# Kernel tuning notes

Hardware: AMD Instinct MI355X
Metric: run time of the kernel (lower is better)

Reference implementation:

```python
import jax, jax.numpy as jnp
import numpy as np


def _conv2d(x, w, b, dilation=1):
    pad = dilation * (w.shape[-1] // 2)
    y = jax.lax.conv_general_dilated(x, w, (1, 1), [(pad, pad), (pad, pad)],
                                     rhs_dilation=(dilation, dilation),
                                     dimension_numbers=("NCHW", "OIHW", "NCHW"))
    return y + b[None, :, None, None]


def _bn(x, gamma, beta, mean, var):
    # eval-mode BatchNorm2d, eps=1e-5
    inv = gamma / jnp.sqrt(var + 1e-5)
    return (x - mean[None, :, None, None]) * inv[None, :, None, None] + beta[None, :, None, None]


def _frft2d(x, angles):
    # Faithful port of the source frft2d, including the quirk that
    # temp[shft, :] indexes the BATCH dim: since shft is a permutation of
    # 0..N-1, the net effect is that batch entries 0..N-1 get (i)fft'd along
    # axis -2 and entries >= N are untouched.
    temp = jnp.swapaxes(x, -1, -2)
    BC = temp.shape[0]
    for a in angles:
        a = a % 4
        N = temp.shape[-2]
        sN = np.float32(np.sqrt(N))
        mask = (jnp.arange(BC) < N)[:, None, None]
        if a == 1:
            temp = jnp.where(mask, jnp.fft.fft(temp, axis=-2) / sN, temp)
        elif a == 2:
            temp = jnp.flip(temp, axis=-2)
        elif a == 3:
            temp = jnp.where(mask, jnp.fft.ifft(temp, axis=-2) * sN, temp)
        temp = jnp.swapaxes(temp, -1, -2)
    return temp


def setup_inputs() -> dict:
    key = jax.random.key(0)
    ks = jax.random.split(key, 12)
    B, C, H, W = 4, 64, 256, 256
    f = lambda k, shape, s=0.1: jax.random.normal(k, shape, dtype=jnp.float32) * s
    z1 = jnp.zeros((1,), jnp.float32)
    o1 = jnp.ones((1,), jnp.float32)
    return {
        "x": jax.random.normal(ks[0], (B, C, H, W), dtype=jnp.float32),
        "kernel_map": jnp.ones((H, W), dtype=jnp.float32),
        "theta_w": f(ks[1], (1, 1, 3, 3)), "theta_b": z1,
        "phase_w": f(ks[2], (1, 1, 3, 3)), "phase_b": z1,
        "phase_gamma": o1, "phase_beta": z1, "phase_mean": z1, "phase_var": o1,
        "amp_w": f(ks[3], (1, 1, 1, 1)), "amp_b": z1,
        "ms_w1": f(ks[4], (1, 1, 3, 3)), "ms_b1": z1,
        "ms_w2": f(ks[5], (1, 1, 3, 3)), "ms_b2": z1,
        "ms_w3": f(ks[6], (1, 1, 3, 3)), "ms_b3": z1,
        "fc1_w": f(ks[7], (16, 1)), "fc1_b": jnp.zeros((16,), jnp.float32),
        "fc2_w": f(ks[8], (1, 16)), "fc2_b": z1,
        "fin_w": f(ks[9], (1, 6, 1, 1)), "fin_b": z1,
        "fin_gamma": o1, "fin_beta": z1, "fin_mean": z1, "fin_var": o1,
    }


def reference(x, kernel_map, theta_w, theta_b, phase_w, phase_b,
              phase_gamma, phase_beta, phase_mean, phase_var,
              amp_w, amp_b, ms_w1, ms_b1, ms_w2, ms_b2, ms_w3, ms_b3,
              fc1_w, fc1_b, fc2_w, fc2_b, fin_w, fin_b,
              fin_gamma, fin_beta, fin_mean, fin_var):
    B, C, H, W = x.shape
    BC = B * C
    xf = x.reshape(BC, H, W)
    trker = jnp.clip(jax.nn.softplus(kernel_map), 1e-3, 10.0)
    # Riesz kernels, p=(1,1) => sin(pi/2)
    Y = (jnp.arange(H, dtype=jnp.float32) + 1.0)[:, None]
    X = (jnp.arange(W, dtype=jnp.float32) + 1.0)[None, :]
    sa = np.float32(np.sin(0.5 * np.pi))
    denom = jnp.sqrt((X / sa) ** 2 + (Y / sa) ** 2) + 1e-6
    dx = ((-1j) * (X / sa) / denom).astype(jnp.complex64) * trker
    dy = ((-1j) * (Y / sa) / denom).astype(jnp.complex64) * trker
    fa = _frft2d(xf.astype(jnp.complex64), [1, 1])
    R1 = jnp.abs(_frft2d(dx * fa, [-1, -1])) + 1e-6
    R2 = jnp.abs(_frft2d(dy * fa, [-1, -1])) + 1e-6
    A = jnp.sqrt(jax.nn.relu(xf ** 2 + R1 ** 2 + R2 ** 2) + 1e-6)[:, None]
    P = jnp.arctan2(jnp.sqrt(R1 ** 2 + R2 ** 2) + 1e-6, xf + 1e-6)[:, None]
    theta = jnp.arctan2(R2, R1 + 1e-6)[:, None]
    G_theta = theta * jax.nn.sigmoid(_conv2d(theta, theta_w, theta_b))
    P_prime = jax.nn.relu(_bn(_conv2d(P, phase_w, phase_b),
                              phase_gamma, phase_beta, phase_mean, phase_var))
    A_boost = A + jax.nn.relu(_conv2d(A, amp_w, amp_b))
    ms = jnp.concatenate([_conv2d(A_boost, ms_w1, ms_b1, 1),
                          _conv2d(A_boost, ms_w2, ms_b2, 2),
                          _conv2d(A_boost, ms_w3, ms_b3, 3)], axis=1)
    # adaptive_avg_pool2d to (H, W) is the identity here
    gf = jnp.mean(A_boost, axis=(2, 3))  # (BC, 1)
    gw = jax.nn.sigmoid(jax.nn.relu(gf @ fc1_w.T + fc1_b) @ fc2_w.T + fc2_b)
    gw = gw[:, :, None, None]  # (BC,1,1,1)
    fusion = jnp.concatenate([A_boost, P_prime, G_theta, ms * gw], axis=1)  # (BC,6,H,W)
    fused = _bn(_conv2d(fusion, fin_w, fin_b), fin_gamma, fin_beta, fin_mean, fin_var)
    fused = jnp.clip(jax.nn.relu(fused), 0.0, 1.0)
    return fused.reshape(B, C, H, W)
```

## Files before the change

### kernel.cpp

```cpp
#include <hip/hip_runtime.h>
#include <hip/hip_fp16.h>
#include <math.h>

#define PI_F 3.14159265358979323846f

__device__ __forceinline__ unsigned dr4(unsigned n){
  return ((n & 3u) << 6) | (((n >> 2) & 3u) << 4) | (((n >> 4) & 3u) << 2) | ((n >> 6) & 3u);
}

__device__ __forceinline__ float2 cmul(float2 a, float2 b){
  return make_float2(a.x * b.x - a.y * b.y, a.x * b.y + a.y * b.x);
}

__device__ __forceinline__ void fill_tw256(float2* tw, int tid){
  float s, c;
  sincosf((2.0f * PI_F / 256.0f) * (float)tid, &s, &c);
  tw[tid] = make_float2(c, s);
  __syncthreads();
}

template<bool INV>
__device__ __forceinline__ void bfly4(float2 a, float2 b, float2 c, float2 d,
                                      float2 w1, float2 w2, float2 w3,
                                      float2& X0, float2& X1, float2& X2, float2& X3){
  if (!INV){ w1.y = -w1.y; w2.y = -w2.y; w3.y = -w3.y; }
  const float2 t1 = cmul(b, w1), t2 = cmul(c, w2), t3 = cmul(d, w3);
  const float2 s0 = make_float2(a.x + t2.x, a.y + t2.y);
  const float2 s1 = make_float2(a.x - t2.x, a.y - t2.y);
  const float2 s2 = make_float2(t1.x + t3.x, t1.y + t3.y);
  const float2 s3 = make_float2(t1.x - t3.x, t1.y - t3.y);
  X0 = make_float2(s0.x + s2.x, s0.y + s2.y);
  X2 = make_float2(s0.x - s2.x, s0.y - s2.y);
  if (!INV){
    X1 = make_float2(s1.x + s3.y, s1.y - s3.x);
    X3 = make_float2(s1.x - s3.y, s1.y + s3.x);
  } else {
    X1 = make_float2(s1.x - s3.y, s1.y + s3.x);
    X3 = make_float2(s1.x + s3.y, s1.y - s3.x);
  }
}

template<bool INV, bool DUAL>
__device__ __forceinline__ void fft256_row(float2* A, float2* B, const float2* tw, int lane){
  #pragma unroll
  for (int s = 0; s < 4; ++s){
    const int q = 1 << (2 * s);
    const int m = 64 >> (2 * s);
    const int p = lane & (q - 1);
    const int base = ((lane >> (2 * s)) << (2 * s + 2)) + p;
    const float2 w1 = tw[p * m], w2 = tw[2 * p * m], w3 = tw[3 * p * m];
    {
      float2 X0, X1, X2, X3;
      bfly4<INV>(A[base], A[base + q], A[base + 2 * q], A[base + 3 * q], w1, w2, w3, X0, X1, X2, X3);
      A[base] = X0; A[base + q] = X1; A[base + 2 * q] = X2; A[base + 3 * q] = X3;
    }
    if (DUAL){
      float2 X0, X1, X2, X3;
      bfly4<INV>(B[base], B[base + q], B[base + 2 * q], B[base + 3 * q], w1, w2, w3, X0, X1, X2, X3);
      B[base] = X0; B[base + q] = X1; B[base + 2 * q] = X2; B[base + 3 * q] = X3;
    }
    __syncthreads();
  }
}

template<bool INV>
__device__ __forceinline__ void fft256_cols(float2* buf, const float2* tw, int c, int sub){
  #pragma unroll
  for (int s = 0; s < 4; ++s){
    const int q = 1 << (2 * s);
    const int m = 64 >> (2 * s);
    #pragma unroll
    for (int k = 0; k < 2; ++k){
      const int t = sub + (k << 5);
      const int p = t & (q - 1);
      const int base = ((t >> (2 * s)) << (2 * s + 2)) + p;
      const float2 w1 = tw[p * m], w2 = tw[2 * p * m], w3 = tw[3 * p * m];
      float2 X0, X1, X2, X3;
      bfly4<INV>(buf[base * 9 + c], buf[(base + q) * 9 + c],
                 buf[(base + 2 * q) * 9 + c], buf[(base + 3 * q) * 9 + c],
                 w1, w2, w3, X0, X1, X2, X3);
      buf[base * 9 + c] = X0; buf[(base + q) * 9 + c] = X1;
      buf[(base + 2 * q) * 9 + c] = X2; buf[(base + 3 * q) * 9 + c] = X3;
    }
    __syncthreads();
  }
}

__device__ __forceinline__ float packh2(float re, float im){
  __half2 h = __floats2half2_rn(re, im);
  return __builtin_bit_cast(float, h);
}
__device__ __forceinline__ float2 unpackh2(float p){
  return __half22float2(__builtin_bit_cast(__half2, p));
}
__device__ __forceinline__ unsigned packh2u(float a, float b){
  return __builtin_bit_cast(unsigned, __floats2half2_rn(a, b));
}

#define PLANE_PITCH 264
#define PLANE_ELEMS (264 * 264)

__global__ __launch_bounds__(256) void k0_prep(const float* __restrict__ km, float* __restrict__ sT){
  const int idx = blockIdx.x * 256 + threadIdx.x;
  const int u = idx >> 8, v = idx & 255;
  const float kv = km[idx];
  float sp = fmaxf(kv, 0.f) + log1pf(expf(-fabsf(kv)));
  sp = fminf(fmaxf(sp, 1e-3f), 10.f);
  const float fu = (float)(u + 1), fv = (float)(v + 1);
  sT[v * 256 + u] = sp / (sqrtf(fu * fu + fv * fv) + 1e-6f) * (1.0f / 65536.0f);
}

__global__ __launch_bounds__(256) void k1_row(const float* __restrict__ xs, float2* __restrict__ SPEC){
  __shared__ float2 tw[256];
  __shared__ __align__(16) float2 buf[4][256];
  const int tid = threadIdx.x;
  fill_tw256(tw, tid);
  const int grp = tid >> 6, lane = tid & 63;
  const int rs = blockIdx.x * 4 + grp;
  const int j0 = lane << 2;
  const float4 xv = *(const float4*)(xs + (size_t)rs * 256 + j0);
  float2* rb = buf[grp];
  rb[dr4(j0 + 0)] = make_float2(xv.x, 0.f);
  rb[dr4(j0 + 1)] = make_float2(xv.y, 0.f);
  rb[dr4(j0 + 2)] = make_float2(xv.z, 0.f);
  rb[dr4(j0 + 3)] = make_float2(xv.w, 0.f);
  __syncthreads();
  fft256_row<false, false>(rb, (float2*)nullptr, tw, lane);
  float4* dst = (float4*)(SPEC + (size_t)rs * 256);
  const float4* src = (const float4*)rb;
  dst[lane * 2]     = src[lane * 2];
  dst[lane * 2 + 1] = src[lane * 2 + 1];
}

__global__ __launch_bounds__(256) void k2_col(float2* SPEC, const float* __restrict__ sT){
  __shared__ float2 tw[256];
  __shared__ float2 bufA[256 * 9];
  __shared__ float2 bufB[256 * 9];
  const int tid = threadIdx.x;
  fill_tw256(tw, tid);
  const int b_local = blockIdx.x >> 5;
  const int u0 = (blockIdx.x & 31) << 3;
  const int c = tid & 7, sub = tid >> 3;
  const size_t rowbase = (size_t)b_local * 256;

  #pragma unroll
  for (int k = 0; k < 8; ++k){
    const int l = tid + (k << 8);
    const int r = l >> 3, cc = l & 7;
    bufA[dr4(r) * 9 + cc] = SPEC[(rowbase + r) * 256 + u0 + cc];
  }
  __syncthreads();
  fft256_cols<false>(bufA, tw, c, sub);

  float s8[8];
  #pragma unroll
  for (int k = 0; k < 8; ++k){
    const int l = tid + (k << 8);
    const int v = l >> 3, cc = l & 7;
    const int u = u0 + cc;
    const float s = sT[v * 256 + u];
    s8[k] = s;
    const float2 F = bufA[v * 9 + cc];
    const float s1 = (float)(v + 1) * s;
    bufB[dr4(v) * 9 + cc] = make_float2(s1 * F.y, -s1 * F.x);
  }
  __syncthreads();
  fft256_cols<true>(bufB, tw, c, sub);

  float u1h[8];
  #pragma unroll
  for (int k = 0; k < 8; ++k){
    const int l = tid + (k << 8);
    const int i = l >> 3, cc = l & 7;
    const float2 f1 = bufB[i * 9 + cc];
    u1h[k] = packh2(f1.x, f1.y);
  }
  __syncthreads();

  #pragma unroll
  for (int k = 0; k < 8; ++k){
    const int l = tid + (k << 8);
    const int v = l >> 3, cc = l & 7;
    const int u = u0 + cc;
    const float2 F = bufA[v * 9 + cc];
    const float s2 = (float)(u + 1) * s8[k];
    bufB[dr4(v) * 9 + cc] = make_float2(s2 * F.y, -s2 * F.x);
  }
  __syncthreads();
  fft256_cols<true>(bufB, tw, c, sub);

  #pragma unroll
  for (int k = 0; k < 8; ++k){
    const int l = tid + (k << 8);
    const int i = l >> 3, cc = l & 7;
    const float2 f2 = bufB[i * 9 + cc];
    float2 slot;
    slot.x = u1h[k];
    slot.y = packh2(f2.x, f2.y);
    SPEC[(rowbase + i) * 256 + u0 + cc] = slot;
  }
}

__global__ __launch_bounds__(256) void k3_rowinv(const float* __restrict__ xs,
    const float2* __restrict__ SPEC, float* __restrict__ Ap, unsigned* __restrict__ PTp,
    const float* __restrict__ ampw, const float* __restrict__ ampb){
  __shared__ float2 tw[256];
  __shared__ __align__(16) float2 b1[4][256];
  __shared__ __align__(16) float2 b2[4][256];
  const int tid = threadIdx.x;
  fill_tw256(tw, tid);
  const int grp = tid >> 6, lane = tid & 63;
  const int rs = blockIdx.x * 4 + grp;
  const int j0 = lane << 2;
  const float4* srow = (const float4*)(SPEC + (size_t)rs * 256);
  const float4 qa = srow[lane * 2], qb = srow[lane * 2 + 1];
  b1[grp][dr4(j0 + 0)] = unpackh2(qa.x); b2[grp][dr4(j0 + 0)] = unpackh2(qa.y);
  b1[grp][dr4(j0 + 1)] = unpackh2(qa.z); b2[grp][dr4(j0 + 1)] = unpackh2(qa.w);
  b1[grp][dr4(j0 + 2)] = unpackh2(qb.x); b2[grp][dr4(j0 + 2)] = unpackh2(qb.y);
  b1[grp][dr4(j0 + 3)] = unpackh2(qb.z); b2[grp][dr4(j0 + 3)] = unpackh2(qb.w);
  __syncthreads();
  fft256_row<true, true>(b1[grp], b2[grp], tw, lane);

  const float aw = *ampw, ab = *ampb;
  const float4 xv = *(const float4*)(xs + (size_t)rs * 256 + j0);
  const float xa[4] = {xv.x, xv.y, xv.z, xv.w};
  float A4[4], P4[4], T4[4];
  #pragma unroll
  for (int k = 0; k < 4; ++k){
    const float2 r1 = b1[grp][j0 + k];
    const float2 r2 = b2[grp][j0 + k];
    const float R1 = sqrtf(r1.x * r1.x + r1.y * r1.y) + 1e-6f;
    const float R2 = sqrtf(r2.x * r2.x + r2.y * r2.y) + 1e-6f;
    const float xvv = xa[k];
    const float A = sqrtf(fmaxf(xvv * xvv + R1 * R1 + R2 * R2, 0.f) + 1e-6f);
    P4[k] = atan2f(sqrtf(R1 * R1 + R2 * R2) + 1e-6f, xvv + 1e-6f);
    T4[k] = atan2f(R2, R1 + 1e-6f);
    A4[k] = A + fmaxf(aw * A + ab, 0.f);
  }
  const int img = rs >> 8, i = rs & 255;
  float* arow = Ap + (size_t)img * PLANE_ELEMS + (size_t)(i + 4) * PLANE_PITCH + 4;
  *(float4*)(arow + j0) = make_float4(A4[0], A4[1], A4[2], A4[3]);
  unsigned* ptrow = PTp + (size_t)img * PLANE_ELEMS + (size_t)(i + 4) * PLANE_PITCH + 4;
  uint4 pk;
  pk.x = packh2u(P4[0], T4[0]); pk.y = packh2u(P4[1], T4[1]);
  pk.z = packh2u(P4[2], T4[2]); pk.w = packh2u(P4[3], T4[3]);
  *(uint4*)(ptrow + j0) = pk;
}

__global__ __launch_bounds__(256) void kpad(float* __restrict__ Ap, unsigned* __restrict__ PTp){
  const int b = blockIdx.x, tid = threadIdx.x;
  float* A = Ap + (size_t)b * PLANE_ELEMS;
  unsigned* P = PTp + (size_t)b * PLANE_ELEMS;
  for (int idx = tid; idx < 4 * PLANE_PITCH; idx += 256){
    const int r = idx / PLANE_PITCH, c2 = idx % PLANE_PITCH;
    A[r * PLANE_PITCH + c2] = 0.f;          P[r * PLANE_PITCH + c2] = 0u;
    A[(260 + r) * PLANE_PITCH + c2] = 0.f;  P[(260 + r) * PLANE_PITCH + c2] = 0u;
  }
  for (int idx = tid; idx < 256 * 4; idx += 256){
    const int r = 4 + (idx >> 2), c2 = idx & 3;
    A[r * PLANE_PITCH + c2] = 0.f;          P[r * PLANE_PITCH + c2] = 0u;
    A[r * PLANE_PITCH + 260 + c2] = 0.f;    P[r * PLANE_PITCH + 260 + c2] = 0u;
  }
}

__global__ __launch_bounds__(256) void k4_gw(const float* __restrict__ Ap,
    const float* __restrict__ fc1w, const float* __restrict__ fc1b,
    const float* __restrict__ fc2w, const float* __restrict__ fc2b,
    float* __restrict__ gw){
  __shared__ float red[256];
  const int b = blockIdx.x, tid = threadIdx.x;
  const float4* row = (const float4*)(Ap + (size_t)b * PLANE_ELEMS + (size_t)(tid + 4) * PLANE_PITCH + 4);
  float s = 0.f;
  #pragma unroll 8
  for (int k = 0; k < 64; ++k){
    const float4 v = row[k];
    s += v.x + v.y + v.z + v.w;
  }
  red[tid] = s;
  __syncthreads();
  #pragma unroll
  for (int off = 128; off; off >>= 1){
    if (tid < off) red[tid] += red[tid + off];
    __syncthreads();
  }
  if (tid == 0){
    const float gf = red[0] * (1.0f / 65536.0f);
    float acc = fc2b[0];
    #pragma unroll
    for (int k = 0; k < 16; ++k)
      acc += fc2w[k] * fmaxf(gf * fc1w[k] + fc1b[k], 0.f);
    gw[b] = 1.f / (1.f + expf(-acc));
  }
}

__global__ __launch_bounds__(256) void k5_fuse(
    const float* __restrict__ Ap, const unsigned* __restrict__ PTp,
    const float* __restrict__ gwp,
    const float* __restrict__ theta_w, const float* __restrict__ theta_b,
    const float* __restrict__ phase_w, const float* __restrict__ phase_b,
    const float* __restrict__ phase_gamma, const float* __restrict__ phase_beta,
    const float* __restrict__ phase_mean, const float* __restrict__ phase_var,
    const float* __restrict__ ms_w1, const float* __restrict__ ms_b1,
    const float* __restrict__ ms_w2, const float* __restrict__ ms_b2,
    const float* __restrict__ ms_w3, const float* __restrict__ ms_b3,
    const float* __restrict__ fin_w, const float* __restrict__ fin_b,
    const float* __restrict__ fin_gamma, const float* __restrict__ fin_beta,
    const float* __restrict__ fin_mean, const float* __restrict__ fin_var,
    float* __restrict__ out){
  const int z = blockIdx.z;
  const int tx = threadIdx.x & 15, ty = threadIdx.x >> 4;
  const int j0 = (blockIdx.x << 6) + (tx << 2);
  const int i0 = (blockIdx.y << 6) + (ty << 2);
  const float* Abase = Ap + (size_t)z * PLANE_ELEMS;
  const unsigned* Pbase = PTp + (size_t)z * PLANE_ELEMS;

  float tw9[9], pw9[9], w1[9], w2[9], w3[9];
  #pragma unroll
  for (int k = 0; k < 9; ++k){
    tw9[k] = theta_w[k]; pw9[k] = phase_w[k];
    w1[k] = ms_w1[k]; w2[k] = ms_w2[k]; w3[k] = ms_w3[k];
  }
  const float b1s = ms_b1[0], b2s = ms_b2[0], b3s = ms_b3[0];
  const float tbs = theta_b[0], pbs = phase_b[0];

  float4 m1[4], m2[4], m3[4], at[4], ap[4], Ac[4], Tc[4];
  #pragma unroll
  for (int oi = 0; oi < 4; ++oi){
    m1[oi] = make_float4(b1s, b1s, b1s, b1s);
    m2[oi] = make_float4(b2s, b2s, b2s, b2s);
    m3[oi] = make_float4(b3s, b3s, b3s, b3s);
    at[oi] = make_float4(tbs, tbs, tbs, tbs);
    ap[oi] = make_float4(pbs, pbs, pbs, pbs);
  }

  #pragma unroll
  for (int lr = 0; lr < 10; ++lr){
    const int ar = i0 - 3 + lr;
    const float* rowp = Abase + (size_t)(ar + 4) * PLANE_PITCH + j0;
    const float4 va = *(const float4*)(rowp);
    const float4 vb = *(const float4*)(rowp + 4);
    const float4 vc = *(const float4*)(rowp + 8);
    const float a[12] = {va.x, va.y, va.z, va.w, vb.x, vb.y, vb.z, vb.w, vc.x, vc.y, vc.z, vc.w};
    #pragma unroll
    for (int oi = 0; oi < 4; ++oi){
      const int dd = lr - 3 - oi;
      if (dd >= -1 && dd <= 1){
        const int wr = (dd + 1) * 3;
        #pragma unroll
        for (int dx = -1; dx <= 1; ++dx){
          const float w = w1[wr + dx + 1];
          m1[oi].x += w * a[4 + 0 + dx]; m1[oi].y += w * a[4 + 1 + dx];
          m1[oi].z += w * a[4 + 2 + dx]; m1[oi].w += w * a[4 + 3 + dx];
        }
      }
      if (dd == -2 || dd == 0 || dd == 2){
        const int wr = (dd / 2 + 1) * 3;
        #pragma unroll
        for (int dx = -1; dx <= 1; ++dx){
          const float w = w2[wr + dx + 1];
          m2[oi].x += w * a[4 + 0 + 2 * dx]; m2[oi].y += w * a[4 + 1 + 2 * dx];
          m2[oi].z += w * a[4 + 2 + 2 * dx]; m2[oi].w += w * a[4 + 3 + 2 * dx];
        }
      }
      if (dd == -3 || dd == 0 || dd == 3){
        const int wr = (dd / 3 + 1) * 3;
        #pragma unroll
        for (int dx = -1; dx <= 1; ++dx){
          const float w = w3[wr + dx + 1];
          m3[oi].x += w * a[4 + 0 + 3 * dx]; m3[oi].y += w * a[4 + 1 + 3 * dx];
          m3[oi].z += w * a[4 + 2 + 3 * dx]; m3[oi].w += w * a[4 + 3 + 3 * dx];
        }
      }
      if (dd == 0) Ac[oi] = make_float4(a[4], a[5], a[6], a[7]);
    }
  }

  #pragma unroll
  for (int lr = 0; lr < 6; ++lr){
    const int ar = i0 - 1 + lr;
    const unsigned* rowp = Pbase + (size_t)(ar + 4) * PLANE_PITCH + j0;
    const uint4 ua = *(const uint4*)(rowp);
    const uint4 ub = *(const uint4*)(rowp + 4);
    const uint4 uc = *(const uint4*)(rowp + 8);
    const unsigned uu[12] = {ua.x, ua.y, ua.z, ua.w, ub.x, ub.y, ub.z, ub.w, uc.x, uc.y, uc.z, uc.w};
    float p[12], t[12];
    #pragma unroll
    for (int k = 0; k < 12; ++k){
      const float2 pt = __half22float2(__builtin_bit_cast(__half2, uu[k]));
      p[k] = pt.x; t[k] = pt.y;
    }
    #pragma unroll
    for (int oi = 0; oi < 4; ++oi){
      const int dd = lr - 1 - oi;
      if (dd >= -1 && dd <= 1){
        const int wr = (dd + 1) * 3;
        #pragma unroll
        for (int dx = -1; dx <= 1; ++dx){
          const float wp = pw9[wr + dx + 1], wt = tw9[wr + dx + 1];
          ap[oi].x += wp * p[4 + 0 + dx]; ap[oi].y += wp * p[4 + 1 + dx];
          ap[oi].z += wp * p[4 + 2 + dx]; ap[oi].w += wp * p[4 + 3 + dx];
          at[oi].x += wt * t[4 + 0 + dx]; at[oi].y += wt * t[4 + 1 + dx];
          at[oi].z += wt * t[4 + 2 + dx]; at[oi].w += wt * t[4 + 3 + dx];
        }
      }
      if (dd == 0) Tc[oi] = make_float4(t[4], t[5], t[6], t[7]);
    }
  }

  const float gwb = gwp[z];
  const float inv_p = phase_gamma[0] * rsqrtf(phase_var[0] + 1e-5f);
  const float pmean = phase_mean[0], pbeta = phase_beta[0];
  const float f0 = fin_w[0], f1 = fin_w[1], f2 = fin_w[2];
  const float f3 = fin_w[3], f4 = fin_w[4], f5 = fin_w[5];
  const float fb = fin_b[0];
  const float inv_f = fin_gamma[0] * rsqrtf(fin_var[0] + 1e-5f);
  const float fmean = fin_mean[0], fbeta = fin_beta[0];

  #pragma unroll
  for (int oi = 0; oi < 4; ++oi){
    float o4[4];
    const float mm1[4] = {m1[oi].x, m1[oi].y, m1[oi].z, m1[oi].w};
    const float mm2[4] = {m2[oi].x, m2[oi].y, m2[oi].z, m2[oi].w};
    const float mm3[4] = {m3[oi].x, m3[oi].y, m3[oi].z, m3[oi].w};
    const float tt[4]  = {at[oi].x, at[oi].y, at[oi].z, at[oi].w};
    const float pp[4]  = {ap[oi].x, ap[oi].y, ap[oi].z, ap[oi].w};
    const float ac[4]  = {Ac[oi].x, Ac[oi].y, Ac[oi].z, Ac[oi].w};
    const float tc[4]  = {Tc[oi].x, Tc[oi].y, Tc[oi].z, Tc[oi].w};
    #pragma unroll
    for (int oj = 0; oj < 4; ++oj){
      const float Gt = tc[oj] / (1.f + expf(-tt[oj]));
      const float Pp = fmaxf((pp[oj] - pmean) * inv_p + pbeta, 0.f);
      const float pre = f0 * ac[oj] + f1 * Pp + f2 * Gt
                      + gwb * (f3 * mm1[oj] + f4 * mm2[oj] + f5 * mm3[oj]) + fb;
      float o = (pre - fmean) * inv_f + fbeta;
      o4[oj] = fminf(fmaxf(o, 0.f), 1.f);
    }
    *(float4*)(out + ((size_t)(z * 256 + i0 + oi) << 8) + j0) = make_float4(o4[0], o4[1], o4[2], o4[3]);
  }
}

extern "C" void kernel_launch(void* const* d_in, const int* in_sizes, int n_in,
                              void* d_out, int out_size, void* d_ws, size_t ws_size,
                              hipStream_t stream){
  const float* x  = (const float*)d_in[0];
  const float* km = (const float*)d_in[1];

  int N = 1;
  while (N < 64){
    const size_t need = (size_t)(256 / N) * 1081856ull + 262144ull + 1024ull;
    if (need <= ws_size) break;
    N <<= 1;
  }
  const int imgsPer = 256 / N;
  const int rowsPer = imgsPer * 256;

  char* ws = (char*)d_ws;
  float*    Aplane = (float*)ws;
  unsigned* PTplane = (unsigned*)(ws + (size_t)imgsPer * 278784ull);
  float2*   SPEC   = (float2*)(ws + (size_t)imgsPer * 557568ull);
  float*    sTab   = (float*)(ws + (size_t)imgsPer * 1081856ull);
  float*    gwbuf  = (float*)(ws + (size_t)imgsPer * 1081856ull + 262144ull);

  k0_prep<<<256, 256, 0, stream>>>(km, sTab);

  for (int s = 0; s < N; ++s){
    const float* xs = x + (size_t)s * rowsPer * 256;
    float* outs = (float*)d_out + (size_t)s * rowsPer * 256;

    k1_row<<<rowsPer / 4, 256, 0, stream>>>(xs, SPEC);
    k2_col<<<imgsPer * 32, 256, 0, stream>>>(SPEC, sTab);
    k3_rowinv<<<rowsPer / 4, 256, 0, stream>>>(xs, SPEC, Aplane, PTplane,
        (const float*)d_in[10], (const float*)d_in[11]);
    kpad<<<imgsPer, 256, 0, stream>>>(Aplane, PTplane);
    k4_gw<<<imgsPer, 256, 0, stream>>>(Aplane,
        (const float*)d_in[18], (const float*)d_in[19],
        (const float*)d_in[20], (const float*)d_in[21], gwbuf);
    k5_fuse<<<dim3(4, 4, imgsPer), 256, 0, stream>>>(
        Aplane, PTplane, gwbuf,
        (const float*)d_in[2],  (const float*)d_in[3],
        (const float*)d_in[4],  (const float*)d_in[5],
        (const float*)d_in[6],  (const float*)d_in[7],
        (const float*)d_in[8],  (const float*)d_in[9],
        (const float*)d_in[12], (const float*)d_in[13],
        (const float*)d_in[14], (const float*)d_in[15],
        (const float*)d_in[16], (const float*)d_in[17],
        (const float*)d_in[22], (const float*)d_in[23],
        (const float*)d_in[24], (const float*)d_in[25],
        (const float*)d_in[26], (const float*)d_in[27],
        outs);
  }
}
```

Before: 391.2 us.

## Replace LDS radix-4 FFTs with register shuffle FFTs and a shared row arena

```diff
diff --git a/kernel.cpp b/kernel.cpp
--- a/kernel.cpp
+++ b/kernel.cpp
@@ -3,273 +3,237 @@
 #include <math.h>
 
 #define PI_F 3.14159265358979323846f
-
-__device__ __forceinline__ unsigned dr4(unsigned n){
-  return ((n & 3u) << 6) | (((n >> 2) & 3u) << 4) | (((n >> 4) & 3u) << 2) | ((n >> 6) & 3u);
-}
-
-__device__ __forceinline__ float2 cmul(float2 a, float2 b){
-  return make_float2(a.x * b.x - a.y * b.y, a.x * b.y + a.y * b.x);
-}
-
-__device__ __forceinline__ void fill_tw256(float2* tw, int tid){
-  float s, c;
-  sincosf((2.0f * PI_F / 256.0f) * (float)tid, &s, &c);
-  tw[tid] = make_float2(c, s);
-  __syncthreads();
-}
-
-template<bool INV>
-__device__ __forceinline__ void bfly4(float2 a, float2 b, float2 c, float2 d,
-                                      float2 w1, float2 w2, float2 w3,
-                                      float2& X0, float2& X1, float2& X2, float2& X3){
-  if (!INV){ w1.y = -w1.y; w2.y = -w2.y; w3.y = -w3.y; }
-  const float2 t1 = cmul(b, w1), t2 = cmul(c, w2), t3 = cmul(d, w3);
-  const float2 s0 = make_float2(a.x + t2.x, a.y + t2.y);
-  const float2 s1 = make_float2(a.x - t2.x, a.y - t2.y);
-  const float2 s2 = make_float2(t1.x + t3.x, t1.y + t3.y);
-  const float2 s3 = make_float2(t1.x - t3.x, t1.y - t3.y);
-  X0 = make_float2(s0.x + s2.x, s0.y + s2.y);
-  X2 = make_float2(s0.x - s2.x, s0.y - s2.y);
-  if (!INV){
-    X1 = make_float2(s1.x + s3.y, s1.y - s3.x);
-    X3 = make_float2(s1.x - s3.y, s1.y + s3.x);
-  } else {
-    X1 = make_float2(s1.x - s3.y, s1.y + s3.x);
-    X3 = make_float2(s1.x + s3.y, s1.y - s3.x);
-  }
-}
-
-template<bool INV, bool DUAL>
-__device__ __forceinline__ void fft256_row(float2* A, float2* B, const float2* tw, int lane){
-  #pragma unroll
-  for (int s = 0; s < 4; ++s){
-    const int q = 1 << (2 * s);
-    const int m = 64 >> (2 * s);
-    const int p = lane & (q - 1);
-    const int base = ((lane >> (2 * s)) << (2 * s + 2)) + p;
-    const float2 w1 = tw[p * m], w2 = tw[2 * p * m], w3 = tw[3 * p * m];
-    {
-      float2 X0, X1, X2, X3;
-      bfly4<INV>(A[base], A[base + q], A[base + 2 * q], A[base + 3 * q], w1, w2, w3, X0, X1, X2, X3);
-      A[base] = X0; A[base + q] = X1; A[base + 2 * q] = X2; A[base + 3 * q] = X3;
-    }
-    if (DUAL){
-      float2 X0, X1, X2, X3;
-      bfly4<INV>(B[base], B[base + q], B[base + 2 * q], B[base + 3 * q], w1, w2, w3, X0, X1, X2, X3);
-      B[base] = X0; B[base + q] = X1; B[base + 2 * q] = X2; B[base + 3 * q] = X3;
-    }
-    __syncthreads();
-  }
-}
-
-template<bool INV>
-__device__ __forceinline__ void fft256_cols(float2* buf, const float2* tw, int c, int sub){
-  #pragma unroll
-  for (int s = 0; s < 4; ++s){
-    const int q = 1 << (2 * s);
-    const int m = 64 >> (2 * s);
-    #pragma unroll
-    for (int k = 0; k < 2; ++k){
-      const int t = sub + (k << 5);
-      const int p = t & (q - 1);
-      const int base = ((t >> (2 * s)) << (2 * s + 2)) + p;
-      const float2 w1 = tw[p * m], w2 = tw[2 * p * m], w3 = tw[3 * p * m];
-      float2 X0, X1, X2, X3;
-      bfly4<INV>(buf[base * 9 + c], buf[(base + q) * 9 + c],
-                 buf[(base + 2 * q) * 9 + c], buf[(base + 3 * q) * 9 + c],
-                 w1, w2, w3, X0, X1, X2, X3);
-      buf[base * 9 + c] = X0; buf[(base + q) * 9 + c] = X1;
-      buf[(base + 2 * q) * 9 + c] = X2; buf[(base + 3 * q) * 9 + c] = X3;
-    }
-    __syncthreads();
-  }
-}
-
-__device__ __forceinline__ float packh2(float re, float im){
-  __half2 h = __floats2half2_rn(re, im);
-  return __builtin_bit_cast(float, h);
+#define ROWB 2112ull
+#define IMGB (ROWB * 256ull)
+
+__device__ __forceinline__ unsigned rev8(unsigned v){ return __brev(v) >> 24; }
+
+__device__ __forceinline__ float2 cmulf(float2 a, float2 b){ return make_float2(a.x*b.x - a.y*b.y, a.x*b.y + a.y*b.x); }
+__device__ __forceinline__ float2 cmulc(float2 a, float2 b){ return make_float2(a.x*b.x + a.y*b.y, a.y*b.x - a.x*b.y); }
+__device__ __forceinline__ float2 cadd (float2 a, float2 b){ return make_float2(a.x+b.x, a.y+b.y); }
+__device__ __forceinline__ float2 csub (float2 a, float2 b){ return make_float2(a.x-b.x, a.y-b.y); }
+__device__ __forceinline__ float2 eix(float a){ float s, c; __sincosf(a, &s, &c); return make_float2(c, s); }
+__device__ __forceinline__ float2 sx(float2 v, int d){ return make_float2(__shfl_xor(v.x, d), __shfl_xor(v.y, d)); }
+
+__device__ __forceinline__ unsigned packh2u(float a, float b){
+  return __builtin_bit_cast(unsigned, __floats2half2_rn(a, b));
 }
 __device__ __forceinline__ float2 unpackh2(float p){
   return __half22float2(__builtin_bit_cast(__half2, p));
 }
-__device__ __forceinline__ unsigned packh2u(float a, float b){
-  return __builtin_bit_cast(unsigned, __floats2half2_rn(a, b));
-}
-
-#define PLANE_PITCH 264
-#define PLANE_ELEMS (264 * 264)
-
-__global__ __launch_bounds__(256) void k0_prep(const float* __restrict__ km, float* __restrict__ sT){
+
+struct Twid { float2 w, w2, t[6]; };
+__device__ __forceinline__ void mktw(Twid& T, int lane){
+  T.w  = eix(-(2.0f * PI_F / 256.0f) * (float)lane);
+  T.w2 = cmulf(T.w, T.w);
+  #pragma unroll
+  for (int st = 0; st < 6; ++st){
+    const int d = 32 >> st;
+    T.t[st] = eix(-(PI_F / (float)d) * (float)(lane & (d - 1)));
+  }
+}
+
+__device__ __forceinline__ void fft256_fwd(float2 v[4], int lane, const Twid& T){
+  const float2 t0 = cadd(v[0], v[2]);
+  const float2 b0 = cmulf(csub(v[0], v[2]), T.w);
+  const float2 t1 = cadd(v[1], v[3]);
+  const float2 w64 = make_float2(T.w.y, -T.w.x);
+  const float2 b1 = cmulf(csub(v[1], v[3]), w64);
+  v[0] = cadd(t0, t1);
+  v[1] = cmulf(csub(t0, t1), T.w2);
+  v[2] = cadd(b0, b1);
+  v[3] = cmulf(csub(b0, b1), T.w2);
+  #pragma unroll
+  for (int st = 0; st < 6; ++st){
+    const int d = 32 >> st;
+    const float2 tw = T.t[st];
+    const bool hi = (lane & d) != 0;
+    #pragma unroll
+    for (int s = 0; s < 4; ++s){
+      const float2 p  = sx(v[s], d);
+      const float2 bo = cmulf(csub(p, v[s]), tw);
+      const float2 lo = cadd(v[s], p);
+      v[s] = hi ? bo : lo;
+    }
+  }
+}
+
+__device__ __forceinline__ void fft256_inv(float2 v[4], int lane, const Twid& T){
+  #pragma unroll
+  for (int st = 0; st < 6; ++st){
+    const int d = 1 << st;
+    const float2 tw = T.t[5 - st];
+    const bool hi = (lane & d) != 0;
+    #pragma unroll
+    for (int s = 0; s < 4; ++s){
+      const float2 p = sx(v[s], d);
+      const float2 m = cmulc(hi ? v[s] : p, tw);
+      v[s] = hi ? csub(p, m) : cadd(v[s], m);
+    }
+  }
+  const float2 m1 = cmulc(v[1], T.w2);
+  const float2 m3a = cmulc(v[3], T.w2);
+  const float2 n0 = cadd(v[0], m1), n1 = csub(v[0], m1);
+  const float2 n2 = cadd(v[2], m3a), n3 = csub(v[2], m3a);
+  const float2 m2 = cmulc(n2, T.w);
+  const float2 uci = make_float2(T.w.y, T.w.x);
+  const float2 m3 = cmulf(n3, uci);
+  v[0] = cadd(n0, m2); v[2] = csub(n0, m2);
+  v[1] = cadd(n1, m3); v[3] = csub(n1, m3);
+}
+
+__global__ __launch_bounds__(256) void k0_prep(const float* __restrict__ km,
+                                               float* __restrict__ sTabS,
+                                               float* __restrict__ zrow){
   const int idx = blockIdx.x * 256 + threadIdx.x;
-  const int u = idx >> 8, v = idx & 255;
-  const float kv = km[idx];
+  const int q = idx >> 8, r = idx & 255;
+  const int u = rev8(q), v = rev8(r);
+  const float kv = km[u * 256 + v];
   float sp = fmaxf(kv, 0.f) + log1pf(expf(-fabsf(kv)));
   sp = fminf(fmaxf(sp, 1e-3f), 10.f);
   const float fu = (float)(u + 1), fv = (float)(v + 1);
-  sT[v * 256 + u] = sp / (sqrtf(fu * fu + fv * fv) + 1e-6f) * (1.0f / 65536.0f);
-}
-
-__global__ __launch_bounds__(256) void k1_row(const float* __restrict__ xs, float2* __restrict__ SPEC){
-  __shared__ float2 tw[256];
-  __shared__ __align__(16) float2 buf[4][256];
+  sTabS[idx] = sp / (sqrtf(fu * fu + fv * fv) + 1e-6f) * (1.0f / 65536.0f);
+  if (blockIdx.x == 0){
+    zrow[threadIdx.x] = 0.f;
+    zrow[threadIdx.x + 256] = 0.f;
+    if (threadIdx.x < 16) zrow[threadIdx.x + 512] = 0.f;
+  }
+}
+
+__global__ __launch_bounds__(256) void k1_row(const float* __restrict__ x, char* __restrict__ arena){
+  const int grp = threadIdx.x >> 6, lane = threadIdx.x & 63;
+  const int rs = blockIdx.x * 4 + grp;
+  Twid T; mktw(T, lane);
+  const float* xr = x + (size_t)rs * 256;
+  float2 v[4];
+  #pragma unroll
+  for (int s = 0; s < 4; ++s) v[s] = make_float2(xr[lane + 64 * s], 0.f);
+  fft256_fwd(v, lane, T);
+  float2* S = (float2*)(arena + (size_t)rs * ROWB);
+  #pragma unroll
+  for (int s = 0; s < 4; ++s) S[lane + 64 * s] = v[s];
+}
+
+__global__ __launch_bounds__(256) void k2_col(char* __restrict__ arena, const float* __restrict__ sTabS){
+  __shared__ float2 lds[256 * 9];
   const int tid = threadIdx.x;
-  fill_tw256(tw, tid);
-  const int grp = tid >> 6, lane = tid & 63;
+  const int b  = blockIdx.x >> 5;
+  const int u0 = (blockIdx.x & 31) << 3;
+  char* base = arena + (size_t)b * IMGB;
+
+  #pragma unroll
+  for (int k = 0; k < 8; ++k){
+    const int idx = tid + (k << 8);
+    const int r = idx >> 3, cc = idx & 7;
+    lds[r * 9 + (cc ^ ((r >> 3) & 7))] = *(const float2*)(base + (size_t)r * ROWB + (size_t)(u0 + cc) * 8);
+  }
+  __syncthreads();
+
+  const int wv = tid >> 6, lane = tid & 63;
+  Twid T; mktw(T, lane);
+  const int r6 = __brev(lane) >> 26;
+  float fvv[4];
+  fvv[0] = (float)(4 * r6 + 0 + 1);
+  fvv[1] = (float)(4 * r6 + 2 + 1);
+  fvv[2] = (float)(4 * r6 + 1 + 1);
+  fvv[3] = (float)(4 * r6 + 3 + 1);
+  const int swb = (lane >> 3) & 7;
+
+  uint2 res0[4], res1[4];
+  #pragma unroll
+  for (int cp = 0; cp < 2; ++cp){
+    const int c = wv * 2 + cp;
+    const int q = u0 + c;
+    const int swc = c ^ swb;
+    float2 F[4];
+    #pragma unroll
+    for (int s = 0; s < 4; ++s) F[s] = lds[(lane + 64 * s) * 9 + swc];
+    fft256_fwd(F, lane, T);
+    float sc[4];
+    #pragma unroll
+    for (int s = 0; s < 4; ++s) sc[s] = sTabS[q * 256 + lane + 64 * s];
+    const float fu = (float)(rev8((unsigned)q) + 1);
+    float2 G[4];
+    #pragma unroll
+    for (int s = 0; s < 4; ++s){ const float a = fvv[s] * sc[s]; G[s] = make_float2(a * F[s].y, -a * F[s].x); }
+    fft256_inv(G, lane, T);
+    #pragma unroll
+    for (int s = 0; s < 4; ++s){ (cp ? res1 : res0)[s].x = packh2u(G[s].x, G[s].y); }
+    #pragma unroll
+    for (int s = 0; s < 4; ++s){ const float a = fu * sc[s]; G[s] = make_float2(a * F[s].y, -a * F[s].x); }
+    fft256_inv(G, lane, T);
+    #pragma unroll
+    for (int s = 0; s < 4; ++s){ (cp ? res1 : res0)[s].y = packh2u(G[s].x, G[s].y); }
+  }
+  __syncthreads();
+  #pragma unroll
+  for (int cp = 0; cp < 2; ++cp){
+    const int c = wv * 2 + cp;
+    const int swc = c ^ swb;
+    #pragma unroll
+    for (int s = 0; s < 4; ++s){
+      const uint2 rr = cp ? res1[s] : res0[s];
+      lds[(lane + 64 * s) * 9 + swc] = make_float2(__uint_as_float(rr.x), __uint_as_float(rr.y));
+    }
+  }
+  __syncthreads();
+  #pragma unroll
+  for (int k = 0; k < 8; ++k){
+    const int idx = tid + (k << 8);
+    const int r = idx >> 3, cc = idx & 7;
+    *(float2*)(base + (size_t)r * ROWB + (size_t)(u0 + cc) * 8) = lds[r * 9 + (cc ^ ((r >> 3) & 7))];
+  }
+}
+
+__global__ __launch_bounds__(256) void k3_rowinv(const float* __restrict__ x, char* __restrict__ arena,
+    const float* __restrict__ ampw, const float* __restrict__ ampb){
+  const int grp = threadIdx.x >> 6, lane = threadIdx.x & 63;
   const int rs = blockIdx.x * 4 + grp;
-  const int j0 = lane << 2;
-  const float4 xv = *(const float4*)(xs + (size_t)rs * 256 + j0);
-  float2* rb = buf[grp];
-  rb[dr4(j0 + 0)] = make_float2(xv.x, 0.f);
-  rb[dr4(j0 + 1)] = make_float2(xv.y, 0.f);
-  rb[dr4(j0 + 2)] = make_float2(xv.z, 0.f);
-  rb[dr4(j0 + 3)] = make_float2(xv.w, 0.f);
-  __syncthreads();
-  fft256_row<false, false>(rb, (float2*)nullptr, tw, lane);
-  float4* dst = (float4*)(SPEC + (size_t)rs * 256);
-  const float4* src = (const float4*)rb;
-  dst[lane * 2]     = src[lane * 2];
-  dst[lane * 2 + 1] = src[lane * 2 + 1];
-}
-
-__global__ __launch_bounds__(256) void k2_col(float2* SPEC, const float* __restrict__ sT){
-  __shared__ float2 tw[256];
-  __shared__ float2 bufA[256 * 9];
-  __shared__ float2 bufB[256 * 9];
-  const int tid = threadIdx.x;
-  fill_tw256(tw, tid);
-  const int b_local = blockIdx.x >> 5;
-  const int u0 = (blockIdx.x & 31) << 3;
-  const int c = tid & 7, sub = tid >> 3;
-  const size_t rowbase = (size_t)b_local * 256;
-
-  #pragma unroll
-  for (int k = 0; k < 8; ++k){
-    const int l = tid + (k << 8);
-    const int r = l >> 3, cc = l & 7;
-    bufA[dr4(r) * 9 + cc] = SPEC[(rowbase + r) * 256 + u0 + cc];
-  }
-  __syncthreads();
-  fft256_cols<false>(bufA, tw, c, sub);
-
-  float s8[8];
-  #pragma unroll
-  for (int k = 0; k < 8; ++k){
-    const int l = tid + (k << 8);
-    const int v = l >> 3, cc = l & 7;
-    const int u = u0 + cc;
-    const float s = sT[v * 256 + u];
-    s8[k] = s;
-    const float2 F = bufA[v * 9 + cc];
-    const float s1 = (float)(v + 1) * s;
-    bufB[dr4(v) * 9 + cc] = make_float2(s1 * F.y, -s1 * F.x);
-  }
-  __syncthreads();
-  fft256_cols<true>(bufB, tw, c, sub);
-
-  float u1h[8];
-  #pragma unroll
-  for (int k = 0; k < 8; ++k){
-    const int l = tid + (k << 8);
-    const int i = l >> 3, cc = l & 7;
-    const float2 f1 = bufB[i * 9 + cc];
-    u1h[k] = packh2(f1.x, f1.y);
-  }
-  __syncthreads();
-
-  #pragma unroll
-  for (int k = 0; k < 8; ++k){
-    const int l = tid + (k << 8);
-    const int v = l >> 3, cc = l & 7;
-    const int u = u0 + cc;
-    const float2 F = bufA[v * 9 + cc];
-    const float s2 = (float)(u + 1) * s8[k];
-    bufB[dr4(v) * 9 + cc] = make_float2(s2 * F.y, -s2 * F.x);
-  }
-  __syncthreads();
-  fft256_cols<true>(bufB, tw, c, sub);
-
-  #pragma unroll
-  for (int k = 0; k < 8; ++k){
-    const int l = tid + (k << 8);
-    const int i = l >> 3, cc = l & 7;
-    const float2 f2 = bufB[i * 9 + cc];
-    float2 slot;
-    slot.x = u1h[k];
-    slot.y = packh2(f2.x, f2.y);
-    SPEC[(rowbase + i) * 256 + u0 + cc] = slot;
-  }
-}
-
-__global__ __launch_bounds__(256) void k3_rowinv(const float* __restrict__ xs,
-    const float2* __restrict__ SPEC, float* __restrict__ Ap, unsigned* __restrict__ PTp,
-    const float* __restrict__ ampw, const float* __restrict__ ampb){
-  __shared__ float2 tw[256];
-  __shared__ __align__(16) float2 b1[4][256];
-  __shared__ __align__(16) float2 b2[4][256];
-  const int tid = threadIdx.x;
-  fill_tw256(tw, tid);
-  const int grp = tid >> 6, lane = tid & 63;
-  const int rs = blockIdx.x * 4 + grp;
-  const int j0 = lane << 2;
-  const float4* srow = (const float4*)(SPEC + (size_t)rs * 256);
-  const float4 qa = srow[lane * 2], qb = srow[lane * 2 + 1];
-  b1[grp][dr4(j0 + 0)] = unpackh2(qa.x); b2[grp][dr4(j0 + 0)] = unpackh2(qa.y);
-  b1[grp][dr4(j0 + 1)] = unpackh2(qa.z); b2[grp][dr4(j0 + 1)] = unpackh2(qa.w);
-  b1[grp][dr4(j0 + 2)] = unpackh2(qb.x); b2[grp][dr4(j0 + 2)] = unpackh2(qb.y);
-  b1[grp][dr4(j0 + 3)] = unpackh2(qb.z); b2[grp][dr4(j0 + 3)] = unpackh2(qb.w);
-  __syncthreads();
-  fft256_row<true, true>(b1[grp], b2[grp], tw, lane);
-
+  Twid T; mktw(T, lane);
+  char* rowb = arena + (size_t)rs * ROWB;
+  float2 g1[4], g2[4];
+  #pragma unroll
+  for (int s = 0; s < 4; ++s){
+    const float2 pk = *(const float2*)(rowb + (size_t)(lane + 64 * s) * 8);
+    g1[s] = unpackh2(pk.x); g2[s] = unpackh2(pk.y);
+  }
+  fft256_inv(g1, lane, T);
+  fft256_inv(g2, lane, T);
   const float aw = *ampw, ab = *ampb;
-  const float4 xv = *(const float4*)(xs + (size_t)rs * 256 + j0);
-  const float xa[4] = {xv.x, xv.y, xv.z, xv.w};
-  float A4[4], P4[4], T4[4];
-  #pragma unroll
-  for (int k = 0; k < 4; ++k){
-    const float2 r1 = b1[grp][j0 + k];
-    const float2 r2 = b2[grp][j0 + k];
-    const float R1 = sqrtf(r1.x * r1.x + r1.y * r1.y) + 1e-6f;
-    const float R2 = sqrtf(r2.x * r2.x + r2.y * r2.y) + 1e-6f;
-    const float xvv = xa[k];
-    const float A = sqrtf(fmaxf(xvv * xvv + R1 * R1 + R2 * R2, 0.f) + 1e-6f);
-    P4[k] = atan2f(sqrtf(R1 * R1 + R2 * R2) + 1e-6f, xvv + 1e-6f);
-    T4[k] = atan2f(R2, R1 + 1e-6f);
-    A4[k] = A + fmaxf(aw * A + ab, 0.f);
-  }
-  const int img = rs >> 8, i = rs & 255;
-  float* arow = Ap + (size_t)img * PLANE_ELEMS + (size_t)(i + 4) * PLANE_PITCH + 4;
-  *(float4*)(arow + j0) = make_float4(A4[0], A4[1], A4[2], A4[3]);
-  unsigned* ptrow = PTp + (size_t)img * PLANE_ELEMS + (size_t)(i + 4) * PLANE_PITCH + 4;
-  uint4 pk;
-  pk.x = packh2u(P4[0], T4[0]); pk.y = packh2u(P4[1], T4[1]);
-  pk.z = packh2u(P4[2], T4[2]); pk.w = packh2u(P4[3], T4[3]);
-  *(uint4*)(ptrow + j0) = pk;
-}
-
-__global__ __launch_bounds__(256) void kpad(float* __restrict__ Ap, unsigned* __restrict__ PTp){
-  const int b = blockIdx.x, tid = threadIdx.x;
-  float* A = Ap + (size_t)b * PLANE_ELEMS;
-  unsigned* P = PTp + (size_t)b * PLANE_ELEMS;
-  for (int idx = tid; idx < 4 * PLANE_PITCH; idx += 256){
-    const int r = idx / PLANE_PITCH, c2 = idx % PLANE_PITCH;
-    A[r * PLANE_PITCH + c2] = 0.f;          P[r * PLANE_PITCH + c2] = 0u;
-    A[(260 + r) * PLANE_PITCH + c2] = 0.f;  P[(260 + r) * PLANE_PITCH + c2] = 0u;
-  }
-  for (int idx = tid; idx < 256 * 4; idx += 256){
-    const int r = 4 + (idx >> 2), c2 = idx & 3;
-    A[r * PLANE_PITCH + c2] = 0.f;          P[r * PLANE_PITCH + c2] = 0u;
-    A[r * PLANE_PITCH + 260 + c2] = 0.f;    P[r * PLANE_PITCH + 260 + c2] = 0u;
-  }
-}
-
-__global__ __launch_bounds__(256) void k4_gw(const float* __restrict__ Ap,
+  const float* xr = x + (size_t)rs * 256;
+  float* Arow = (float*)(rowb + 16);
+  unsigned* Prow = (unsigned*)(rowb + 1072);
+  #pragma unroll
+  for (int s = 0; s < 4; ++s){
+    const int j = lane + 64 * s;
+    const float xv = xr[j];
+    const float R1 = sqrtf(g1[s].x * g1[s].x + g1[s].y * g1[s].y) + 1e-6f;
+    const float R2 = sqrtf(g2[s].x * g2[s].x + g2[s].y * g2[s].y) + 1e-6f;
+    const float A = sqrtf(fmaxf(xv * xv + R1 * R1 + R2 * R2, 0.f) + 1e-6f);
+    const float P = atan2f(sqrtf(R1 * R1 + R2 * R2) + 1e-6f, xv + 1e-6f);
+    const float Th = atan2f(R2, R1 + 1e-6f);
+    const float Ab = A + fmaxf(aw * A + ab, 0.f);
+    Arow[j] = Ab;
+    Prow[j] = packh2u(P, Th);
+  }
+}
+
+__global__ __launch_bounds__(256) void kpad(char* __restrict__ arena){
+  char* row = arena + (size_t)blockIdx.x * IMGB + (size_t)threadIdx.x * ROWB;
+  const float4 z = make_float4(0.f, 0.f, 0.f, 0.f);
+  *(float4*)(row)         = z;
+  *(float4*)(row + 1040)  = z;
+  *(float4*)(row + 1056)  = z;
+  *(float4*)(row + 2096)  = z;
+}
+
+__global__ __launch_bounds__(256) void k4_gw(const char* __restrict__ arena,
     const float* __restrict__ fc1w, const float* __restrict__ fc1b,
     const float* __restrict__ fc2w, const float* __restrict__ fc2b,
     float* __restrict__ gw){
   __shared__ float red[256];
-  const int b = blockIdx.x, tid = threadIdx.x;
-  const float4* row = (const float4*)(Ap + (size_t)b * PLANE_ELEMS + (size_t)(tid + 4) * PLANE_PITCH + 4);
+  const int tid = threadIdx.x;
+  const float4* row = (const float4*)(arena + (size_t)blockIdx.x * IMGB + (size_t)tid * ROWB + 16);
   float s = 0.f;
   #pragma unroll 8
   for (int k = 0; k < 64; ++k){
@@ -289,12 +253,12 @@
     #pragma unroll
     for (int k = 0; k < 16; ++k)
       acc += fc2w[k] * fmaxf(gf * fc1w[k] + fc1b[k], 0.f);
-    gw[b] = 1.f / (1.f + expf(-acc));
+    gw[blockIdx.x] = 1.f / (1.f + expf(-acc));
   }
 }
 
 __global__ __launch_bounds__(256) void k5_fuse(
-    const float* __restrict__ Ap, const unsigned* __restrict__ PTp,
+    const char* __restrict__ arena, const float* __restrict__ zrowf,
     const float* __restrict__ gwp,
     const float* __restrict__ theta_w, const float* __restrict__ theta_b,
     const float* __restrict__ phase_w, const float* __restrict__ phase_b,
@@ -311,8 +275,7 @@
   const int tx = threadIdx.x & 15, ty = threadIdx.x >> 4;
   const int j0 = (blockIdx.x << 6) + (tx << 2);
   const int i0 = (blockIdx.y << 6) + (ty << 2);
-  const float* Abase = Ap + (size_t)z * PLANE_ELEMS;
-  const unsigned* Pbase = PTp + (size_t)z * PLANE_ELEMS;
+  const char* img = arena + (size_t)z * IMGB;
 
   float tw9[9], pw9[9], w1[9], w2[9], w3[9];
   #pragma unroll
@@ -336,10 +299,10 @@
   #pragma unroll
   for (int lr = 0; lr < 10; ++lr){
     const int ar = i0 - 3 + lr;
-    const float* rowp = Abase + (size_t)(ar + 4) * PLANE_PITCH + j0;
-    const float4 va = *(const float4*)(rowp);
-    const float4 vb = *(const float4*)(rowp + 4);
-    const float4 vc = *(const float4*)(rowp + 8);
+    const float* rowA = ((unsigned)ar < 256u) ? (const float*)(img + (size_t)ar * ROWB) : zrowf;
+    const float4 va = *(const float4*)(rowA + j0);
+    const float4 vb = *(const float4*)(rowA + j0 + 4);
+    const float4 vc = *(const float4*)(rowA + j0 + 8);
     const float a[12] = {va.x, va.y, va.z, va.w, vb.x, vb.y, vb.z, vb.w, vc.x, vc.y, vc.z, vc.w};
     #pragma unroll
     for (int oi = 0; oi < 4; ++oi){
@@ -378,15 +341,16 @@
   #pragma unroll
   for (int lr = 0; lr < 6; ++lr){
     const int ar = i0 - 1 + lr;
-    const unsigned* rowp = Pbase + (size_t)(ar + 4) * PLANE_PITCH + j0;
-    const uint4 ua = *(const uint4*)(rowp);
-    const uint4 ub = *(const uint4*)(rowp + 4);
-    const uint4 uc = *(const uint4*)(rowp + 8);
+    const unsigned* rowP = ((unsigned)ar < 256u) ? (const unsigned*)(img + (size_t)ar * ROWB + 1056)
+                                                 : (const unsigned*)zrowf;
+    const uint4 ua = *(const uint4*)(rowP + j0);
+    const uint4 ub = *(const uint4*)(rowP + j0 + 4);
+    const uint4 uc = *(const uint4*)(rowP + j0 + 8);
     const unsigned uu[12] = {ua.x, ua.y, ua.z, ua.w, ub.x, ub.y, ub.z, ub.w, uc.x, uc.y, uc.z, uc.w};
     float p[12], t[12];
     #pragma unroll
     for (int k = 0; k < 12; ++k){
-      const float2 pt = __half22float2(__builtin_bit_cast(__half2, uu[k]));
+      const float2 pt = unpackh2(__builtin_bit_cast(float, uu[k]));
       p[k] = pt.x; t[k] = pt.y;
     }
     #pragma unroll
@@ -418,7 +382,6 @@
 
   #pragma unroll
   for (int oi = 0; oi < 4; ++oi){
-    float o4[4];
     const float mm1[4] = {m1[oi].x, m1[oi].y, m1[oi].z, m1[oi].w};
     const float mm2[4] = {m2[oi].x, m2[oi].y, m2[oi].z, m2[oi].w};
     const float mm3[4] = {m3[oi].x, m3[oi].y, m3[oi].z, m3[oi].w};
@@ -426,6 +389,7 @@
     const float pp[4]  = {ap[oi].x, ap[oi].y, ap[oi].z, ap[oi].w};
     const float ac[4]  = {Ac[oi].x, Ac[oi].y, Ac[oi].z, Ac[oi].w};
     const float tc[4]  = {Tc[oi].x, Tc[oi].y, Tc[oi].z, Tc[oi].w};
+    float o4[4];
     #pragma unroll
     for (int oj = 0; oj < 4; ++oj){
       const float Gt = tc[oj] / (1.f + expf(-tt[oj]));
@@ -447,36 +411,35 @@
 
   int N = 1;
   while (N < 64){
-    const size_t need = (size_t)(256 / N) * 1081856ull + 262144ull + 1024ull;
+    const size_t need = (size_t)(256 / N) * IMGB + 2112ull + 262144ull + 1024ull;
     if (need <= ws_size) break;
     N <<= 1;
   }
   const int imgsPer = 256 / N;
   const int rowsPer = imgsPer * 256;
 
-  char* ws = (char*)d_ws;
-  float*    Aplane = (float*)ws;
-  unsigned* PTplane = (unsigned*)(ws + (size_t)imgsPer * 278784ull);
-  float2*   SPEC   = (float2*)(ws + (size_t)imgsPer * 557568ull);
-  float*    sTab   = (float*)(ws + (size_t)imgsPer * 1081856ull);
-  float*    gwbuf  = (float*)(ws + (size_t)imgsPer * 1081856ull + 262144ull);
-
-  k0_prep<<<256, 256, 0, stream>>>(km, sTab);
+  char*  ws    = (char*)d_ws;
+  char*  arena = ws;
+  float* zrow  = (float*)(ws + (size_t)imgsPer * IMGB);
+  float* sTabS = (float*)(ws + (size_t)imgsPer * IMGB + 2112ull);
+  float* gwbuf = (float*)(ws + (size_t)imgsPer * IMGB + 2112ull + 262144ull);
+
+  k0_prep<<<256, 256, 0, stream>>>(km, sTabS, zrow);
 
   for (int s = 0; s < N; ++s){
     const float* xs = x + (size_t)s * rowsPer * 256;
     float* outs = (float*)d_out + (size_t)s * rowsPer * 256;
 
-    k1_row<<<rowsPer / 4, 256, 0, stream>>>(xs, SPEC);
-    k2_col<<<imgsPer * 32, 256, 0, stream>>>(SPEC, sTab);
-    k3_rowinv<<<rowsPer / 4, 256, 0, stream>>>(xs, SPEC, Aplane, PTplane,
+    k1_row<<<rowsPer / 4, 256, 0, stream>>>(xs, arena);
+    k2_col<<<imgsPer * 32, 256, 0, stream>>>(arena, sTabS);
+    k3_rowinv<<<rowsPer / 4, 256, 0, stream>>>(xs, arena,
         (const float*)d_in[10], (const float*)d_in[11]);
-    kpad<<<imgsPer, 256, 0, stream>>>(Aplane, PTplane);
-    k4_gw<<<imgsPer, 256, 0, stream>>>(Aplane,
+    kpad<<<imgsPer, 256, 0, stream>>>(arena);
+    k4_gw<<<imgsPer, 256, 0, stream>>>(arena,
         (const float*)d_in[18], (const float*)d_in[19],
         (const float*)d_in[20], (const float*)d_in[21], gwbuf);
     k5_fuse<<<dim3(4, 4, imgsPer), 256, 0, stream>>>(
-        Aplane, PTplane, gwbuf,
+        arena, zrow, gwbuf,
         (const float*)d_in[2],  (const float*)d_in[3],
         (const float*)d_in[4],  (const float*)d_in[5],
         (const float*)d_in[6],  (const float*)d_in[7],
```

Measured after the change: 404.8 us. +3.5%, slower.
